# Optimization experiments

Hardware: AMD Instinct MI355X
Metric: run time of the kernel (lower is better)

## Reference

```python
import jax, jax.numpy as jnp
import numpy as np

# -------- problem dimensions (match init_kwargs / input_specs) --------
B, N, D = 4, 16384, 64          # batch, nodes (=128*128 pixels), feature dim
Q = 128                         # plateau/propagation state width (hardcoded in forward)
W = H = 128                     # grid (hardcoded in forward)
E = 131072                      # edges per batch element
M = 4                           # num_masks = k_nodes - 1
NUM_ITERS = 25                  # GraphPropagator(num_iters=25)
ADJ_THRESH = 0.5                # GraphPropagator(adj_thresh=0.5)


def setup_inputs() -> dict:
    key = jax.random.key(0)
    k1, k2, k3, k4 = jax.random.split(key, 4)
    node_features = jax.random.normal(k1, (B, N, D), dtype=jnp.float32)
    # global node indices in [0, B*N) -- the torch code concatenates per-batch
    # edge lists directly into a (B*N, B*N) SparseTensor
    node_edges = jax.random.randint(k2, (B, 2, E), 0, B * N)
    node_weights = jax.random.uniform(k3, (B, E), dtype=jnp.float32)
    init_state = jax.random.normal(k4, (B, N, Q), dtype=jnp.float32)
    return {"node_features": node_features, "node_edges": node_edges,
            "node_weights": node_weights, "init_state": init_state}


def _propagate(init_state, rows, cols, ws):
    """25-iteration sparse label propagation on the global (B*N,B*N) graph."""
    h = init_state.reshape(B * N, Q)

    def step(h, _):
        msg = ws[:, None] * h[cols]                                  # gather  [B*E, Q]
        agg = jax.ops.segment_sum(msg, rows, num_segments=B * N)    # scatter [B*N, Q]
        hn = agg / (jnp.linalg.norm(agg, axis=-1, keepdims=True) + 1e-8)
        return hn, None

    h, _ = jax.lax.scan(step, h, None, length=NUM_ITERS)
    return h  # [B*N, Q]


def _competition(platmap):
    """Competition(num_masks=M): agents claim pixels by plateau-vector affinity;
    an extra zero-logit background channel yields the unharvested mask."""
    flat = platmap.reshape(B, W * H, Q)
    agent_idx = jnp.linspace(0, W * H - 1, M).astype(jnp.int32)      # deterministic agent pixels
    agents = flat[:, agent_idx, :]                                   # [B, M, Q]
    logits = jnp.einsum('bnq,bmq->bnm', flat, agents) / jnp.sqrt(jnp.float32(Q))
    logits_ext = jnp.concatenate([logits, jnp.zeros((B, W * H, 1), logits.dtype)], axis=-1)
    probs = jax.nn.softmax(logits_ext, axis=-1)                      # [B, WH, M+1]
    masks = probs[..., :M].reshape(B, W, H, M)
    unharv = probs[..., M:].reshape(B, W, H, 1)
    alive = jnp.ones((B, M, 1), dtype=platmap.dtype)
    pheno = agents
    return masks, agents, alive, pheno, unharv


def reference(node_features, node_edges, node_weights, init_state):
    rows = node_edges[:, 0, :].reshape(-1)                           # [B*E] global row idx
    cols = node_edges[:, 1, :].reshape(-1)
    ws = node_weights.reshape(-1)
    ws = jnp.where(ws > ADJ_THRESH, ws, jnp.float32(0.0))            # adjacency threshold

    prop = _propagate(init_state, rows, cols, ws)                    # [B*N, Q]
    platmap = prop.reshape(B, W, H, Q)

    masks, agents, alive, pheno, unharv = _competition(platmap)
    masks_ext = jnp.concatenate([masks, unharv], axis=-1)            # [B, W, H, M+1]
    masks_ext = jnp.transpose(masks_ext, (0, 3, 1, 2))               # [B, M+1, W, H]

    nf = jnp.einsum('bnd,bmn->bmd', node_features,
                    masks_ext.reshape(B, M + 1, W * H))              # [B, M+1, D]
    # F.normalize(p=2, dim=1, eps=1e-12)
    nf = nf / jnp.clip(jnp.linalg.norm(nf, axis=1, keepdims=True), 1e-12)
    node_scores = jnp.max(masks_ext, axis=(-1, -2))                  # [B, M+1]
    return nf, masks_ext, node_scores
```

## Files before the change

### kernel.cpp

```cpp
#include <hip/hip_runtime.h>

#define B_    4
#define N_    16384
#define D_    64
#define Q_    128
#define E_    131072
#define M_    4
#define BN    65536
#define TOTE  524288
#define ITERS 25
#define PAD_CAP (TOTE + 3 * BN + 64)

#define OFF_MASKS 1280
#define OFF_SCORES 328960

__constant__ int c_agidx[4] = {0, 5461, 10922, 16383};

__device__ __forceinline__ unsigned pack_bf16x2(float x, float y) {
    unsigned ux = __float_as_uint(x);
    unsigned uy = __float_as_uint(y);
    ux = (ux + 0x7fffu + ((ux >> 16) & 1u)) >> 16;
    uy = (uy + 0x7fffu + ((uy >> 16) & 1u)) & 0xffff0000u;
    return ux | uy;
}

__global__ void k_count(const int* __restrict__ edges, const float* __restrict__ wts,
                        int* __restrict__ deg) {
    int idx = blockIdx.x * blockDim.x + threadIdx.x;
    if (idx >= TOTE) return;
    int b = idx >> 17;
    int e = idx & (E_ - 1);
    float w = wts[idx];
    if (w > 0.5f) {
        int row = edges[(b * 2) * E_ + e];
        atomicAdd(&deg[row], 1);
    }
}

__global__ void k_scan(const int* __restrict__ deg, int* __restrict__ row_start) {
    __shared__ int sums[1024];
    int t = threadIdx.x;
    int base = t * 64;
    int s = 0;
    for (int i = 0; i < 64; ++i) s += (deg[base + i] + 3) & ~3;
    sums[t] = s;
    __syncthreads();
    for (int off = 1; off < 1024; off <<= 1) {
        int v = sums[t];
        int add = (t >= off) ? sums[t - off] : 0;
        __syncthreads();
        sums[t] = v + add;
        __syncthreads();
    }
    int run = (t == 0) ? 0 : sums[t - 1];
    for (int i = 0; i < 64; ++i) {
        int d = (deg[base + i] + 3) & ~3;
        row_start[base + i] = run;
        run += d;
    }
    if (t == 1023) row_start[BN] = run;
}

__global__ void k_cursor(const int* __restrict__ row_start, int* __restrict__ cursor) {
    int i = blockIdx.x * blockDim.x + threadIdx.x;
    if (i < BN) cursor[i] = row_start[i];
}

__global__ void k_scatter(const int* __restrict__ edges, const float* __restrict__ wts,
                          int* __restrict__ cursor, int2* __restrict__ cw) {
    int idx = blockIdx.x * blockDim.x + threadIdx.x;
    if (idx >= TOTE) return;
    int b = idx >> 17;
    int e = idx & (E_ - 1);
    float w = wts[idx];
    if (w > 0.5f) {
        int row = edges[(b * 2) * E_ + e];
        int col = edges[(b * 2) * E_ + E_ + e];
        int pos = atomicAdd(&cursor[row], 1);
        cw[pos] = make_int2(col, __float_as_int(w));
    }
}

__global__ void k_sort(const int* __restrict__ row_start, const int* __restrict__ deg,
                       int2* __restrict__ cw) {
    int n = blockIdx.x * blockDim.x + threadIdx.x;
    if (n >= BN) return;
    int s = row_start[n], epos = s + deg[n], pend = row_start[n + 1];
    for (int i = s + 1; i < epos; ++i) {
        int2 v = cw[i];
        unsigned long long key =
            ((unsigned long long)(unsigned)v.x << 32) | (unsigned)v.y;
        int j = i - 1;
        while (j >= s) {
            int2 u = cw[j];
            unsigned long long kj =
                ((unsigned long long)(unsigned)u.x << 32) | (unsigned)u.y;
            if (kj <= key) break;
            cw[j + 1] = u;
            --j;
        }
        cw[j + 1] = v;
    }
    for (int i = epos; i < pend; ++i) cw[i] = make_int2(0, 0);
}

__global__ __launch_bounds__(256) void k_cvt(const float* __restrict__ in,
                                             unsigned* __restrict__ out) {
    int i = blockIdx.x * blockDim.x + threadIdx.x;
    float2 v = ((const float2*)in)[i];
    out[i] = pack_bf16x2(v.x, v.y);
}

__global__ __launch_bounds__(256) void k_prop(const unsigned* __restrict__ hin,
                                              unsigned* __restrict__ hout,
                                              const int* __restrict__ row_start,
                                              const int2* __restrict__ cw) {
    int lane = threadIdx.x & 63;
    int node = (blockIdx.x << 2) + (threadIdx.x >> 6);
    int unode = __builtin_amdgcn_readfirstlane(node);
    int s = row_start[unode];
    int e = row_start[unode + 1];
    float ax = 0.f, ay = 0.f;
    for (int i = s; i < e; i += 4) {
        const int4* q = (const int4*)(cw + i);
        int4 a = q[0];
        int4 b = q[1];
        unsigned v0 = hin[((size_t)a.x << 6) + lane];
        unsigned v1 = hin[((size_t)a.z << 6) + lane];
        unsigned v2 = hin[((size_t)b.x << 6) + lane];
        unsigned v3 = hin[((size_t)b.z << 6) + lane];
        float w0 = __int_as_float(a.y), w1 = __int_as_float(a.w);
        float w2 = __int_as_float(b.y), w3 = __int_as_float(b.w);
        ax = fmaf(w0, __uint_as_float(v0 << 16), ax);
        ay = fmaf(w0, __uint_as_float(v0 & 0xffff0000u), ay);
        ax = fmaf(w1, __uint_as_float(v1 << 16), ax);
        ay = fmaf(w1, __uint_as_float(v1 & 0xffff0000u), ay);
        ax = fmaf(w2, __uint_as_float(v2 << 16), ax);
        ay = fmaf(w2, __uint_as_float(v2 & 0xffff0000u), ay);
        ax = fmaf(w3, __uint_as_float(v3 << 16), ax);
        ay = fmaf(w3, __uint_as_float(v3 & 0xffff0000u), ay);
    }
    float ss = ax * ax + ay * ay;
    #pragma unroll
    for (int off = 32; off; off >>= 1) ss += __shfl_xor(ss, off, 64);
    float inv = 1.0f / (sqrtf(ss) + 1e-8f);
    hout[((size_t)unode << 6) + lane] = pack_bf16x2(ax * inv, ay * inv);
}

__global__ __launch_bounds__(256) void k_masks(const unsigned* __restrict__ h,
                                               float* __restrict__ masks) {
    int wave = threadIdx.x >> 6;
    int lane = threadIdx.x & 63;
    int n = blockIdx.x * 4 + wave;
    int b = n >> 14;
    int nl = n & (N_ - 1);
    unsigned vp = h[((size_t)n << 6) + lane];
    float vx = __uint_as_float(vp << 16);
    float vy = __uint_as_float(vp & 0xffff0000u);
    float dot[4];
    #pragma unroll
    for (int m = 0; m < 4; ++m) {
        int an = b * N_ + c_agidx[m];
        unsigned ap = h[((size_t)an << 6) + lane];
        float axx = __uint_as_float(ap << 16);
        float ayy = __uint_as_float(ap & 0xffff0000u);
        float d = vx * axx + vy * ayy;
        #pragma unroll
        for (int off = 32; off; off >>= 1) d += __shfl_xor(d, off, 64);
        dot[m] = d;
    }
    const float scl = 0.0883883476483184405501055452631f;
    float l0 = dot[0] * scl, l1 = dot[1] * scl, l2 = dot[2] * scl, l3 = dot[3] * scl;
    float mx = fmaxf(fmaxf(fmaxf(l0, l1), fmaxf(l2, l3)), 0.f);
    float e0 = expf(l0 - mx), e1 = expf(l1 - mx), e2 = expf(l2 - mx),
          e3 = expf(l3 - mx), e4 = expf(0.f - mx);
    float den = e0 + e1 + e2 + e3 + e4;
    if (lane < 5) {
        float p = (lane == 0) ? e0 : (lane == 1) ? e1 : (lane == 2) ? e2
                  : (lane == 3) ? e3 : e4;
        masks[((size_t)b * 5 + lane) * N_ + nl] = p / den;
    }
}

__global__ __launch_bounds__(256) void k_nfpart(const float* __restrict__ feat,
                                                const float* __restrict__ masks,
                                                float* __restrict__ part,
                                                float* __restrict__ maxpart) {
    int bm = blockIdx.x >> 6;
    int chunk = blockIdx.x & 63;
    int b = bm / 5;
    int d = threadIdx.x & 63;
    int g = threadIdx.x >> 6;
    int n0 = chunk * 256 + g * 64;
    const float* fb = feat + (size_t)b * N_ * D_;
    const float* mk = masks + (size_t)bm * N_;
    float acc = 0.f;
    float mxv = -1e30f;
    for (int i = 0; i < 64; ++i) {
        int n = n0 + i;
        float mv = mk[n];
        acc = fmaf(fb[(size_t)n * D_ + d], mv, acc);
        mxv = fmaxf(mxv, mv);
    }
    __shared__ float lds[4][64];
    __shared__ float lmx[4];
    lds[g][d] = acc;
    if (d == 0) lmx[g] = mxv;
    __syncthreads();
    if (g == 0) {
        float s = lds[0][d] + lds[1][d] + lds[2][d] + lds[3][d];
        part[(size_t)blockIdx.x * 64 + d] = s;
        if (d == 0)
            maxpart[blockIdx.x] = fmaxf(fmaxf(lmx[0], lmx[1]), fmaxf(lmx[2], lmx[3]));
    }
}

__global__ void k_nffinal(const float* __restrict__ part, const float* __restrict__ maxpart,
                          float* __restrict__ out) {
    int b = blockIdx.x;
    int d = threadIdx.x;
    float v[5];
    float ss = 0.f;
    for (int m = 0; m < 5; ++m) {
        int bm = b * 5 + m;
        float s = 0.f;
        for (int c = 0; c < 64; ++c) s += part[(size_t)(bm * 64 + c) * 64 + d];
        v[m] = s;
        ss += s * s;
    }
    float nrm = fmaxf(sqrtf(ss), 1e-12f);
    for (int m = 0; m < 5; ++m) out[((size_t)b * 5 + m) * 64 + d] = v[m] / nrm;
    if (d < 5) {
        int bm = b * 5 + d;
        float mx = -1e30f;
        for (int c = 0; c < 64; ++c) mx = fmaxf(mx, maxpart[bm * 64 + c]);
        out[OFF_SCORES + bm] = mx;
    }
}

extern "C" void kernel_launch(void* const* d_in, const int* in_sizes, int n_in,
                              void* d_out, int out_size, void* d_ws, size_t ws_size,
                              hipStream_t stream) {
    const float* feat  = (const float*)d_in[0];
    const int*   edges = (const int*)d_in[1];
    const float* wts   = (const float*)d_in[2];
    const float* init  = (const float*)d_in[3];
    float* out = (float*)d_out;

    unsigned* hA = (unsigned*)d_ws;
    unsigned* hB = hA + (size_t)BN * 64;
    int* row_start = (int*)(hB + (size_t)BN * 64);
    int* cursor    = row_start + 65544;
    int* deg       = cursor + BN;
    int2* cw       = (int2*)(deg + BN);
    float* part    = (float*)(cw + PAD_CAP);
    float* maxpart = part + 81920;

    hipMemsetAsync(deg, 0, BN * sizeof(int), stream);
    k_count<<<TOTE / 256, 256, 0, stream>>>(edges, wts, deg);
    k_scan<<<1, 1024, 0, stream>>>(deg, row_start);
    k_cursor<<<BN / 256, 256, 0, stream>>>(row_start, cursor);
    k_scatter<<<TOTE / 256, 256, 0, stream>>>(edges, wts, cursor, cw);
    k_sort<<<BN / 256, 256, 0, stream>>>(row_start, deg, cw);

    k_cvt<<<BN * 64 / 256, 256, 0, stream>>>(init, hA);

    const unsigned* src = hA;
    for (int it = 0; it < ITERS; ++it) {
        unsigned* dst = (it & 1) ? hA : hB;
        k_prop<<<BN / 4, 256, 0, stream>>>(src, dst, row_start, cw);
        src = dst;
    }

    k_masks<<<BN / 4, 256, 0, stream>>>(src, out + OFF_MASKS);
    k_nfpart<<<20 * 64, 256, 0, stream>>>(feat, out + OFF_MASKS, part, maxpart);
    k_nffinal<<<4, 64, 0, stream>>>(part, maxpart, out);
}
```

Baseline: 617.7 us.

## Parallelize degree scan, fuse fp32 init into first propagation, unroll gather by 8

Replaces the single-block serial prefix scan with a three-kernel multi-block scan that also writes the cursor, which removes the separate cursor-copy kernel. The bf16 conversion kernel is dropped: the first propagation iteration reads the fp32 initial state directly through a templated gather. The propagation inner loop now handles 8 edges per iteration, putting more independent gathers in flight, with a 4-edge tail loop. Costs are extra launches for the scan and more register use in the unrolled loop. The first iteration now reads fp32 state rather than rounded bf16, which changes numerics slightly.

```diff
diff --git a/kernel.cpp b/kernel.cpp
--- a/kernel.cpp
+++ b/kernel.cpp
@@ -37,33 +37,64 @@
     }
 }
 
-__global__ void k_scan(const int* __restrict__ deg, int* __restrict__ row_start) {
-    __shared__ int sums[1024];
+__global__ __launch_bounds__(256) void k_scan1(const int* __restrict__ deg,
+                                               int* __restrict__ blockSums) {
+    int i = blockIdx.x * 256 + threadIdx.x;
+    int v = (deg[i] + 3) & ~3;
+    #pragma unroll
+    for (int off = 1; off < 64; off <<= 1) v += __shfl_xor(v, off, 64);
+    __shared__ int ws[4];
+    int lane = threadIdx.x & 63, w = threadIdx.x >> 6;
+    if (lane == 0) ws[w] = v;
+    __syncthreads();
+    if (threadIdx.x == 0)
+        blockSums[blockIdx.x] = ws[0] + ws[1] + ws[2] + ws[3];
+}
+
+__global__ __launch_bounds__(256) void k_scan2(const int* __restrict__ blockSums,
+                                               int* __restrict__ blockOffs,
+                                               int* __restrict__ row_start) {
     int t = threadIdx.x;
-    int base = t * 64;
-    int s = 0;
-    for (int i = 0; i < 64; ++i) s += (deg[base + i] + 3) & ~3;
-    sums[t] = s;
+    int lane = t & 63, w = t >> 6;
+    int v = blockSums[t];
+    int incl = v;
+    #pragma unroll
+    for (int off = 1; off < 64; off <<= 1) {
+        int u = __shfl_up(incl, off, 64);
+        if (lane >= off) incl += u;
+    }
+    __shared__ int wtot[4];
+    if (lane == 63) wtot[w] = incl;
     __syncthreads();
-    for (int off = 1; off < 1024; off <<= 1) {
-        int v = sums[t];
-        int add = (t >= off) ? sums[t - off] : 0;
-        __syncthreads();
-        sums[t] = v + add;
-        __syncthreads();
-    }
-    int run = (t == 0) ? 0 : sums[t - 1];
-    for (int i = 0; i < 64; ++i) {
-        int d = (deg[base + i] + 3) & ~3;
-        row_start[base + i] = run;
-        run += d;
-    }
-    if (t == 1023) row_start[BN] = run;
-}
-
-__global__ void k_cursor(const int* __restrict__ row_start, int* __restrict__ cursor) {
-    int i = blockIdx.x * blockDim.x + threadIdx.x;
-    if (i < BN) cursor[i] = row_start[i];
+    int wadd = 0;
+    for (int j = 0; j < w; ++j) wadd += wtot[j];
+    incl += wadd;
+    blockOffs[t] = incl - v;
+    if (t == 255) row_start[BN] = incl;
+}
+
+__global__ __launch_bounds__(256) void k_scan3(const int* __restrict__ deg,
+                                               const int* __restrict__ blockOffs,
+                                               int* __restrict__ row_start,
+                                               int* __restrict__ cursor) {
+    int t = threadIdx.x;
+    int lane = t & 63, w = t >> 6;
+    int i = blockIdx.x * 256 + t;
+    int v = (deg[i] + 3) & ~3;
+    int incl = v;
+    #pragma unroll
+    for (int off = 1; off < 64; off <<= 1) {
+        int u = __shfl_up(incl, off, 64);
+        if (lane >= off) incl += u;
+    }
+    __shared__ int wtot[4];
+    if (lane == 63) wtot[w] = incl;
+    __syncthreads();
+    int wadd = 0;
+    for (int j = 0; j < w; ++j) wadd += wtot[j];
+    int rs = blockOffs[blockIdx.x] + wadd + incl - v;
+    row_start[i] = rs;
+    cursor[i] = rs;
 }
 
 __global__ void k_scatter(const int* __restrict__ edges, const float* __restrict__ wts,
@@ -104,14 +135,8 @@
     for (int i = epos; i < pend; ++i) cw[i] = make_int2(0, 0);
 }
 
-__global__ __launch_bounds__(256) void k_cvt(const float* __restrict__ in,
-                                             unsigned* __restrict__ out) {
-    int i = blockIdx.x * blockDim.x + threadIdx.x;
-    float2 v = ((const float2*)in)[i];
-    out[i] = pack_bf16x2(v.x, v.y);
-}
-
-__global__ __launch_bounds__(256) void k_prop(const unsigned* __restrict__ hin,
+template <bool F32IN>
+__global__ __launch_bounds__(256) void k_prop(const void* __restrict__ hin,
                                               unsigned* __restrict__ hout,
                                               const int* __restrict__ row_start,
                                               const int2* __restrict__ cw) {
@@ -121,24 +146,61 @@
     int s = row_start[unode];
     int e = row_start[unode + 1];
     float ax = 0.f, ay = 0.f;
-    for (int i = s; i < e; i += 4) {
+
+    auto gather = [&](int col) -> float2 {
+        if constexpr (F32IN) {
+            return ((const float2*)hin)[((size_t)col << 6) + lane];
+        } else {
+            unsigned p = ((const unsigned*)hin)[((size_t)col << 6) + lane];
+            float2 r;
+            r.x = __uint_as_float(p << 16);
+            r.y = __uint_as_float(p & 0xffff0000u);
+            return r;
+        }
+    };
+
+    int i = s;
+    for (; i + 8 <= e; i += 8) {
         const int4* q = (const int4*)(cw + i);
         int4 a = q[0];
         int4 b = q[1];
-        unsigned v0 = hin[((size_t)a.x << 6) + lane];
-        unsigned v1 = hin[((size_t)a.z << 6) + lane];
-        unsigned v2 = hin[((size_t)b.x << 6) + lane];
-        unsigned v3 = hin[((size_t)b.z << 6) + lane];
+        int4 c = q[2];
+        int4 d = q[3];
+        float2 v0 = gather(a.x);
+        float2 v1 = gather(a.z);
+        float2 v2 = gather(b.x);
+        float2 v3 = gather(b.z);
+        float2 v4 = gather(c.x);
+        float2 v5 = gather(c.z);
+        float2 v6 = gather(d.x);
+        float2 v7 = gather(d.z);
         float w0 = __int_as_float(a.y), w1 = __int_as_float(a.w);
         float w2 = __int_as_float(b.y), w3 = __int_as_float(b.w);
-        ax = fmaf(w0, __uint_as_float(v0 << 16), ax);
-        ay = fmaf(w0, __uint_as_float(v0 & 0xffff0000u), ay);
-        ax = fmaf(w1, __uint_as_float(v1 << 16), ax);
-        ay = fmaf(w1, __uint_as_float(v1 & 0xffff0000u), ay);
-        ax = fmaf(w2, __uint_as_float(v2 << 16), ax);
-        ay = fmaf(w2, __uint_as_float(v2 & 0xffff0000u), ay);
-        ax = fmaf(w3, __uint_as_float(v3 << 16), ax);
-        ay = fmaf(w3, __uint_as_float(v3 & 0xffff0000u), ay);
+        float w4 = __int_as_float(c.y), w5 = __int_as_float(c.w);
+        float w6 = __int_as_float(d.y), w7 = __int_as_float(d.w);
+        ax = fmaf(w0, v0.x, ax); ay = fmaf(w0, v0.y, ay);
+        ax = fmaf(w1, v1.x, ax); ay = fmaf(w1, v1.y, ay);
+        ax = fmaf(w2, v2.x, ax); ay = fmaf(w2, v2.y, ay);
+        ax = fmaf(w3, v3.x, ax); ay = fmaf(w3, v3.y, ay);
+        ax = fmaf(w4, v4.x, ax); ay = fmaf(w4, v4.y, ay);
+        ax = fmaf(w5, v5.x, ax); ay = fmaf(w5, v5.y, ay);
+        ax = fmaf(w6, v6.x, ax); ay = fmaf(w6, v6.y, ay);
+        ax = fmaf(w7, v7.x, ax); ay = fmaf(w7, v7.y, ay);
+    }
+    for (; i < e; i += 4) {
+        const int4* q = (const int4*)(cw + i);
+        int4 a = q[0];
+        int4 b = q[1];
+        float2 v0 = gather(a.x);
+        float2 v1 = gather(a.z);
+        float2 v2 = gather(b.x);
+        float2 v3 = gather(b.z);
+        float w0 = __int_as_float(a.y), w1 = __int_as_float(a.w);
+        float w2 = __int_as_float(b.y), w3 = __int_as_float(b.w);
+        ax = fmaf(w0, v0.x, ax); ay = fmaf(w0, v0.y, ay);
+        ax = fmaf(w1, v1.x, ax); ay = fmaf(w1, v1.y, ay);
+        ax = fmaf(w2, v2.x, ax); ay = fmaf(w2, v2.y, ay);
+        ax = fmaf(w3, v3.x, ax); ay = fmaf(w3, v3.y, ay);
     }
     float ss = ax * ax + ay * ay;
     #pragma unroll
@@ -249,26 +311,28 @@
 
     unsigned* hA = (unsigned*)d_ws;
     unsigned* hB = hA + (size_t)BN * 64;
-    int* row_start = (int*)(hB + (size_t)BN * 64);
-    int* cursor    = row_start + 65544;
-    int* deg       = cursor + BN;
-    int2* cw       = (int2*)(deg + BN);
-    float* part    = (float*)(cw + PAD_CAP);
-    float* maxpart = part + 81920;
+    int* row_start  = (int*)(hB + (size_t)BN * 64);
+    int* cursor     = row_start + 65544;
+    int* deg        = cursor + BN;
+    int* blockSums  = deg + BN;
+    int* blockOffs  = blockSums + 256;
+    int2* cw        = (int2*)(blockOffs + 256);
+    float* part     = (float*)(cw + PAD_CAP);
+    float* maxpart  = part + 81920;
 
     hipMemsetAsync(deg, 0, BN * sizeof(int), stream);
     k_count<<<TOTE / 256, 256, 0, stream>>>(edges, wts, deg);
-    k_scan<<<1, 1024, 0, stream>>>(deg, row_start);
-    k_cursor<<<BN / 256, 256, 0, stream>>>(row_start, cursor);
+    k_scan1<<<256, 256, 0, stream>>>(deg, blockSums);
+    k_scan2<<<1, 256, 0, stream>>>(blockSums, blockOffs, row_start);
+    k_scan3<<<256, 256, 0, stream>>>(deg, blockOffs, row_start, cursor);
     k_scatter<<<TOTE / 256, 256, 0, stream>>>(edges, wts, cursor, cw);
     k_sort<<<BN / 256, 256, 0, stream>>>(row_start, deg, cw);
 
-    k_cvt<<<BN * 64 / 256, 256, 0, stream>>>(init, hA);
-
+    k_prop<true><<<BN / 4, 256, 0, stream>>>(init, hA, row_start, cw);
     const unsigned* src = hA;
-    for (int it = 0; it < ITERS; ++it) {
-        unsigned* dst = (it & 1) ? hA : hB;
-        k_prop<<<BN / 4, 256, 0, stream>>>(src, dst, row_start, cw);
+    for (int it = 1; it < ITERS; ++it) {
+        unsigned* dst = (it & 1) ? hB : hA;
+        k_prop<false><<<BN / 4, 256, 0, stream>>>(src, dst, row_start, cw);
         src = dst;
     }
 
```

After: 554.8 us. 1.11x faster.
